# Performance work log

Measured on AMD Instinct MI355X. Metric: run time of the kernel, lower is better.

The kernel has to match this reference:

```python
import jax, jax.numpy as jnp
import numpy as np

N = 1048576
D = 128
C = 1000
MOMENTUM = 0.95


def setup_inputs() -> dict:
    key = jax.random.key(0)
    k1, k2, k3, k4 = jax.random.split(key, 4)
    feats = jax.random.normal(k1, (N, D), dtype=jnp.float32)
    labels = jax.random.randint(k2, (N,), 0, C, dtype=jnp.int64)
    weights = jax.random.uniform(k3, (N,), dtype=jnp.float32)
    proto = jax.random.normal(k4, (C, D), dtype=jnp.float32)  # buffer [C, d]
    return {"feats": feats, "labels": labels, "weights": weights, "proto": proto}


def reference(feats, labels, weights, proto):
    # Per-class weighted mean via a single segment reduction (replaces the
    # per-class masked loop in the torch module), then fused EMA update.
    labels = labels.astype(jnp.int32)
    # [C, d] sum of w_i * f_i per class
    wsum_feats = jax.ops.segment_sum(weights[:, None] * feats, labels, num_segments=C)
    # [C] sum of weights per class
    wsum = jax.ops.segment_sum(weights, labels, num_segments=C)
    vec = wsum_feats / jnp.maximum(wsum, 1e-8)[:, None]  # [C, d]
    present = (wsum > 0.0)[:, None]  # classes seen in this batch
    new_proto = jnp.where(present, MOMENTUM * proto + (1.0 - MOMENTUM) * vec, proto)
    return new_proto
```

## Files before the change

### kernel.cpp

```cpp
#include <hip/hip_runtime.h>

#define NROWS 1048576
#define DIM   128
#define NCLS  1000
#define RPB   4096
#define RPT   16
#define MOM   0.95f


__global__ __launch_bounds__(256) void k_hist(const int* __restrict__ labels,
                                              unsigned* __restrict__ total)
{
    __shared__ unsigned h[NCLS];
    const int tid = threadIdx.x;
    for (int c = tid; c < NCLS; c += 256) h[c] = 0u;
    __syncthreads();
    const int base = blockIdx.x * RPB;
#pragma unroll
    for (int k = 0; k < RPT; ++k)
        atomicAdd(&h[labels[base + k * 256 + tid]], 1u);
    __syncthreads();
    for (int c = tid; c < NCLS; c += 256)
        if (h[c]) atomicAdd(&total[c], h[c]);
}

__global__ __launch_bounds__(1024) void k_scan(const unsigned* __restrict__ total,
                                               unsigned* __restrict__ classBase,
                                               unsigned* __restrict__ cursor)
{
    __shared__ unsigned s[1024];
    const int tid = threadIdx.x;
    unsigned v = (tid < NCLS) ? total[tid] : 0u;
    s[tid] = v;
    __syncthreads();
    for (int off = 1; off < 1024; off <<= 1) {
        unsigned u = (tid >= off) ? s[tid - off] : 0u;
        __syncthreads();
        s[tid] += u;
        __syncthreads();
    }
    if (tid < NCLS) {
        unsigned excl = s[tid] - v;
        classBase[tid] = excl;
        cursor[tid]    = excl;
    }
}

__global__ __launch_bounds__(256) void k_scatter(const int* __restrict__ labels,
                                                 unsigned* __restrict__ cursor,
                                                 unsigned* __restrict__ perm)
{
    __shared__ unsigned h[NCLS];
    __shared__ unsigned basec[NCLS];
    const int tid = threadIdx.x;
    for (int c = tid; c < NCLS; c += 256) h[c] = 0u;
    __syncthreads();
    const int base = blockIdx.x * RPB;
    int lab[RPT];
#pragma unroll
    for (int k = 0; k < RPT; ++k) {
        lab[k] = labels[base + k * 256 + tid];
        atomicAdd(&h[lab[k]], 1u);
    }
    __syncthreads();
    for (int c = tid; c < NCLS; c += 256) {
        unsigned cnt = h[c];
        if (cnt) basec[c] = atomicAdd(&cursor[c], cnt);
        h[c] = 0u;
    }
    __syncthreads();
#pragma unroll
    for (int k = 0; k < RPT; ++k) {
        const int c = lab[k];
        unsigned off = atomicAdd(&h[c], 1u);
        perm[basec[c] + off] = (unsigned)(base + k * 256 + tid);
    }
}

__global__ __launch_bounds__(256) void k_reduce(
        const float*    __restrict__ feats,
        const float*    __restrict__ weights,
        const float*    __restrict__ proto,
        const unsigned* __restrict__ perm,
        const unsigned* __restrict__ total,
        const unsigned* __restrict__ classBase,
        float* __restrict__ out)
{
    const int c      = blockIdx.x;
    const int tid    = threadIdx.x;
    const int lane32 = tid & 31;
    const int grp    = tid >> 5;
    const int n      = (int)total[c];
    const unsigned base = classBase[c];
    const float4* __restrict__ f4 = (const float4*)feats;

    float4 acc = make_float4(0.f, 0.f, 0.f, 0.f);
    float  wacc = 0.f;

    int i = grp;
    for (; i + 24 < n; i += 32) {
        unsigned r0 = perm[base + i];
        unsigned r1 = perm[base + i + 8];
        unsigned r2 = perm[base + i + 16];
        unsigned r3 = perm[base + i + 24];
        float w0 = weights[r0], w1 = weights[r1];
        float w2 = weights[r2], w3 = weights[r3];
        float4 f0 = f4[(long)r0 * 32 + lane32];
        float4 f1 = f4[(long)r1 * 32 + lane32];
        float4 f2 = f4[(long)r2 * 32 + lane32];
        float4 f3 = f4[(long)r3 * 32 + lane32];
        acc.x += w0 * f0.x; acc.y += w0 * f0.y; acc.z += w0 * f0.z; acc.w += w0 * f0.w;
        acc.x += w1 * f1.x; acc.y += w1 * f1.y; acc.z += w1 * f1.z; acc.w += w1 * f1.w;
        acc.x += w2 * f2.x; acc.y += w2 * f2.y; acc.z += w2 * f2.z; acc.w += w2 * f2.w;
        acc.x += w3 * f3.x; acc.y += w3 * f3.y; acc.z += w3 * f3.z; acc.w += w3 * f3.w;
        wacc += w0 + w1 + w2 + w3;
    }
    for (; i < n; i += 8) {
        unsigned r = perm[base + i];
        float w = weights[r];
        float4 f = f4[(long)r * 32 + lane32];
        acc.x += w * f.x; acc.y += w * f.y; acc.z += w * f.z; acc.w += w * f.w;
        wacc += w;
    }

    __shared__ float4 sAcc[8][32];
    __shared__ float  sW[8];
    sAcc[grp][lane32] = acc;
    if (lane32 == 0) sW[grp] = wacc;
    __syncthreads();

    if (grp == 0) {
        float4 t = sAcc[0][lane32];
#pragma unroll
        for (int g = 1; g < 8; ++g) {
            float4 a = sAcc[g][lane32];
            t.x += a.x; t.y += a.y; t.z += a.z; t.w += a.w;
        }
        float ws = 0.f;
#pragma unroll
        for (int g = 0; g < 8; ++g) ws += sW[g];

        const float4 p = ((const float4*)proto)[c * 32 + lane32];
        float4 o;
        if (ws > 0.f) {
            const float den = fmaxf(ws, 1e-8f);
            o.x = MOM * p.x + 0.05f * (t.x / den);
            o.y = MOM * p.y + 0.05f * (t.y / den);
            o.z = MOM * p.z + 0.05f * (t.z / den);
            o.w = MOM * p.w + 0.05f * (t.w / den);
        } else {
            o = p;
        }
        ((float4*)out)[c * 32 + lane32] = o;
    }
}

extern "C" void kernel_launch(void* const* d_in, const int* in_sizes, int n_in,
                              void* d_out, int out_size, void* d_ws, size_t ws_size,
                              hipStream_t stream)
{
    const float* feats   = (const float*)d_in[0];
    const int*   labels  = (const int*)  d_in[1];
    const float* weights = (const float*)d_in[2];
    const float* proto   = (const float*)d_in[3];
    float* out = (float*)d_out;

    unsigned* total     = (unsigned*)d_ws;
    unsigned* classBase = total + 1024;
    unsigned* cursor    = classBase + 1024;
    unsigned* perm      = cursor + 1024;

    hipMemsetAsync(total, 0, 1024 * sizeof(unsigned), stream);
    k_hist   <<<256, 256, 0, stream>>>(labels, total);
    k_scan   <<<1, 1024, 0, stream>>>(total, classBase, cursor);
    k_scatter<<<256, 256, 0, stream>>>(labels, cursor, perm);
    k_reduce <<<NCLS, 256, 0, stream>>>(feats, weights, proto, perm,
                                        total, classBase, out);
}
```

Before: 716.1 us.

## Precompute per-block class offsets and widen reduce kernel with deeper unrolling

The histogram kernel now stores each block's per-class counts. A new per-class scan kernel turns those counts into per-block base offsets, so the scatter kernel no longer rebuilds its local histogram or takes global atomics on a shared cursor. Rows are then placed in block order, which gives deterministic ordering and roughly ascending row indices within each class. The reduce kernel moves to 512 threads (16 row groups) and unrolls 8 gathered loads per iteration, so more memory requests are in flight during the scattered feature reads. This costs an extra kernel launch, extra workspace traffic for the 256x1024 count and offset tables, and more registers per thread.

```diff
diff --git a/kernel.cpp b/kernel.cpp
--- a/kernel.cpp
+++ b/kernel.cpp
@@ -3,30 +3,35 @@
 #define NROWS 1048576
 #define DIM   128
 #define NCLS  1000
+#define NBLK  256
 #define RPB   4096
 #define RPT   16
 #define MOM   0.95f
 
 
 __global__ __launch_bounds__(256) void k_hist(const int* __restrict__ labels,
-                                              unsigned* __restrict__ total)
+                                              unsigned* __restrict__ total,
+                                              unsigned* __restrict__ blockCnt)
 {
     __shared__ unsigned h[NCLS];
     const int tid = threadIdx.x;
+    const int b   = blockIdx.x;
     for (int c = tid; c < NCLS; c += 256) h[c] = 0u;
     __syncthreads();
-    const int base = blockIdx.x * RPB;
+    const int base = b * RPB;
 #pragma unroll
     for (int k = 0; k < RPT; ++k)
         atomicAdd(&h[labels[base + k * 256 + tid]], 1u);
     __syncthreads();
-    for (int c = tid; c < NCLS; c += 256)
-        if (h[c]) atomicAdd(&total[c], h[c]);
+    for (int c = tid; c < NCLS; c += 256) {
+        const unsigned cnt = h[c];
+        blockCnt[b * 1024 + c] = cnt;
+        if (cnt) atomicAdd(&total[c], cnt);
+    }
 }
 
 __global__ __launch_bounds__(1024) void k_scan(const unsigned* __restrict__ total,
-                                               unsigned* __restrict__ classBase,
-                                               unsigned* __restrict__ cursor)
+                                               unsigned* __restrict__ classBase)
 {
     __shared__ unsigned s[1024];
     const int tid = threadIdx.x;
@@ -39,45 +44,52 @@
         s[tid] += u;
         __syncthreads();
     }
-    if (tid < NCLS) {
-        unsigned excl = s[tid] - v;
-        classBase[tid] = excl;
-        cursor[tid]    = excl;
+    if (tid < NCLS) classBase[tid] = s[tid] - v;
+}
+
+__global__ __launch_bounds__(256) void k_scanB(const unsigned* __restrict__ blockCnt,
+                                               const unsigned* __restrict__ classBase,
+                                               unsigned* __restrict__ blockBase)
+{
+    __shared__ unsigned s[256];
+    const int c = blockIdx.x;
+    const int t = threadIdx.x;
+    unsigned v = blockCnt[t * 1024 + c];
+    s[t] = v;
+    __syncthreads();
+    for (int off = 1; off < 256; off <<= 1) {
+        unsigned u = (t >= off) ? s[t - off] : 0u;
+        __syncthreads();
+        s[t] += u;
+        __syncthreads();
+    }
+    blockBase[t * 1024 + c] = classBase[c] + (s[t] - v);
+}
+
+__global__ __launch_bounds__(256) void k_scatter(const int* __restrict__ labels,
+                                                 const unsigned* __restrict__ blockBase,
+                                                 unsigned* __restrict__ perm)
+{
+    __shared__ unsigned off_lds[NCLS];
+    __shared__ unsigned basec[NCLS];
+    const int tid = threadIdx.x;
+    const int b   = blockIdx.x;
+    for (int c = tid; c < NCLS; c += 256) {
+        basec[c]   = blockBase[b * 1024 + c];
+        off_lds[c] = 0u;
+    }
+    __syncthreads();
+    const int base = b * RPB;
+#pragma unroll
+    for (int k = 0; k < RPT; ++k) {
+        const int r = base + k * 256 + tid;
+        const int c = labels[r];
+        unsigned o = atomicAdd(&off_lds[c], 1u);
+        perm[basec[c] + o] = (unsigned)r;
     }
 }
 
-__global__ __launch_bounds__(256) void k_scatter(const int* __restrict__ labels,
-                                                 unsigned* __restrict__ cursor,
-                                                 unsigned* __restrict__ perm)
-{
-    __shared__ unsigned h[NCLS];
-    __shared__ unsigned basec[NCLS];
-    const int tid = threadIdx.x;
-    for (int c = tid; c < NCLS; c += 256) h[c] = 0u;
-    __syncthreads();
-    const int base = blockIdx.x * RPB;
-    int lab[RPT];
-#pragma unroll
-    for (int k = 0; k < RPT; ++k) {
-        lab[k] = labels[base + k * 256 + tid];
-        atomicAdd(&h[lab[k]], 1u);
-    }
-    __syncthreads();
-    for (int c = tid; c < NCLS; c += 256) {
-        unsigned cnt = h[c];
-        if (cnt) basec[c] = atomicAdd(&cursor[c], cnt);
-        h[c] = 0u;
-    }
-    __syncthreads();
-#pragma unroll
-    for (int k = 0; k < RPT; ++k) {
-        const int c = lab[k];
-        unsigned off = atomicAdd(&h[c], 1u);
-        perm[basec[c] + off] = (unsigned)(base + k * 256 + tid);
-    }
-}
-
-__global__ __launch_bounds__(256) void k_reduce(
+__global__ __launch_bounds__(512) void k_reduce(
         const float*    __restrict__ feats,
         const float*    __restrict__ weights,
         const float*    __restrict__ proto,
@@ -98,24 +110,22 @@
     float  wacc = 0.f;
 
     int i = grp;
-    for (; i + 24 < n; i += 32) {
-        unsigned r0 = perm[base + i];
-        unsigned r1 = perm[base + i + 8];
-        unsigned r2 = perm[base + i + 16];
-        unsigned r3 = perm[base + i + 24];
-        float w0 = weights[r0], w1 = weights[r1];
-        float w2 = weights[r2], w3 = weights[r3];
-        float4 f0 = f4[(long)r0 * 32 + lane32];
-        float4 f1 = f4[(long)r1 * 32 + lane32];
-        float4 f2 = f4[(long)r2 * 32 + lane32];
-        float4 f3 = f4[(long)r3 * 32 + lane32];
-        acc.x += w0 * f0.x; acc.y += w0 * f0.y; acc.z += w0 * f0.z; acc.w += w0 * f0.w;
-        acc.x += w1 * f1.x; acc.y += w1 * f1.y; acc.z += w1 * f1.z; acc.w += w1 * f1.w;
-        acc.x += w2 * f2.x; acc.y += w2 * f2.y; acc.z += w2 * f2.z; acc.w += w2 * f2.w;
-        acc.x += w3 * f3.x; acc.y += w3 * f3.y; acc.z += w3 * f3.z; acc.w += w3 * f3.w;
-        wacc += w0 + w1 + w2 + w3;
+    for (; i + 112 < n; i += 128) {
+        unsigned r[8]; float w[8]; float4 f[8];
+#pragma unroll
+        for (int u = 0; u < 8; ++u) r[u] = perm[base + i + u * 16];
+#pragma unroll
+        for (int u = 0; u < 8; ++u) w[u] = weights[r[u]];
+#pragma unroll
+        for (int u = 0; u < 8; ++u) f[u] = f4[(long)r[u] * 32 + lane32];
+#pragma unroll
+        for (int u = 0; u < 8; ++u) {
+            acc.x += w[u] * f[u].x; acc.y += w[u] * f[u].y;
+            acc.z += w[u] * f[u].z; acc.w += w[u] * f[u].w;
+            wacc  += w[u];
+        }
     }
-    for (; i < n; i += 8) {
+    for (; i < n; i += 16) {
         unsigned r = perm[base + i];
         float w = weights[r];
         float4 f = f4[(long)r * 32 + lane32];
@@ -123,8 +133,8 @@
         wacc += w;
     }
 
-    __shared__ float4 sAcc[8][32];
-    __shared__ float  sW[8];
+    __shared__ float4 sAcc[16][32];
+    __shared__ float  sW[16];
     sAcc[grp][lane32] = acc;
     if (lane32 == 0) sW[grp] = wacc;
     __syncthreads();
@@ -132,13 +142,13 @@
     if (grp == 0) {
         float4 t = sAcc[0][lane32];
 #pragma unroll
-        for (int g = 1; g < 8; ++g) {
+        for (int g = 1; g < 16; ++g) {
             float4 a = sAcc[g][lane32];
             t.x += a.x; t.y += a.y; t.z += a.z; t.w += a.w;
         }
         float ws = 0.f;
 #pragma unroll
-        for (int g = 0; g < 8; ++g) ws += sW[g];
+        for (int g = 0; g < 16; ++g) ws += sW[g];
 
         const float4 p = ((const float4*)proto)[c * 32 + lane32];
         float4 o;
@@ -167,13 +177,15 @@
 
     unsigned* total     = (unsigned*)d_ws;
     unsigned* classBase = total + 1024;
-    unsigned* cursor    = classBase + 1024;
-    unsigned* perm      = cursor + 1024;
+    unsigned* blockCnt  = classBase + 1024;
+    unsigned* blockBase = blockCnt + NBLK * 1024;
+    unsigned* perm      = blockBase + NBLK * 1024;
 
     hipMemsetAsync(total, 0, 1024 * sizeof(unsigned), stream);
-    k_hist   <<<256, 256, 0, stream>>>(labels, total);
-    k_scan   <<<1, 1024, 0, stream>>>(total, classBase, cursor);
-    k_scatter<<<256, 256, 0, stream>>>(labels, cursor, perm);
-    k_reduce <<<NCLS, 256, 0, stream>>>(feats, weights, proto, perm,
+    k_hist   <<<NBLK, 256, 0, stream>>>(labels, total, blockCnt);
+    k_scan   <<<1, 1024, 0, stream>>>(total, classBase);
+    k_scanB  <<<NCLS, 256, 0, stream>>>(blockCnt, classBase, blockBase);
+    k_scatter<<<NBLK, 256, 0, stream>>>(labels, blockBase, perm);
+    k_reduce <<<NCLS, 512, 0, stream>>>(feats, weights, proto, perm,
                                         total, classBase, out);
 }
```

Measured after the change: 729.4 us. Within noise of the previous version (+1.9%).
